# Performance work log

Hardware: AMD Instinct MI355X
Metric: run time of the kernel (lower is better)

Reference implementation:

```python
import jax, jax.numpy as jnp
import numpy as np

N_NODES = 100000
N_EDGES = 3200000
NFEAT, NHID, NCLASS = 512, 128, 40


def _glorot(key, fan_in, fan_out):
    lim = jnp.sqrt(6.0 / (fan_in + fan_out))
    return jax.random.uniform(key, (fan_in, fan_out), jnp.float32, -lim, lim)


def setup_inputs() -> dict:
    key = jax.random.key(0)
    k1, k2, k3, k4, k5 = jax.random.split(key, 5)
    x = jax.random.normal(k1, (N_NODES, NFEAT), jnp.float32)
    edge_index = jax.random.randint(k2, (2, N_EDGES), 0, N_NODES, jnp.int64)
    edge_weight = jax.random.uniform(k3, (N_EDGES,), jnp.float32)
    W1 = _glorot(k4, NFEAT, NHID)
    b1 = jnp.zeros((NHID,), jnp.float32)
    W2 = _glorot(k5, NHID, NCLASS)
    b2 = jnp.zeros((NCLASS,), jnp.float32)
    return {"x": x, "edge_index": edge_index, "edge_weight": edge_weight,
            "W1": W1, "b1": b1, "W2": W2, "b2": b2}


def _gcn_norm(edge_index, edge_weight, num_nodes):
    # add self loops (weight 1), symmetric normalization D^-1/2 A D^-1/2
    loop = jnp.arange(num_nodes, dtype=edge_index.dtype)
    row = jnp.concatenate([edge_index[0], loop])
    col = jnp.concatenate([edge_index[1], loop])
    w = jnp.concatenate([edge_weight, jnp.ones((num_nodes,), edge_weight.dtype)])
    deg = jax.ops.segment_sum(w, col, num_segments=num_nodes)
    dinv = jnp.where(deg > 0, jax.lax.rsqrt(jnp.maximum(deg, 1e-20)), 0.0)
    norm = dinv[row] * w * dinv[col]
    return row, col, norm


def _gcn_conv(h, row, col, norm, W, b, num_nodes):
    h = h @ W                                  # [N, out]
    msg = norm[:, None] * h[row]               # per-edge gather + scale
    out = jax.ops.segment_sum(msg, col, num_segments=num_nodes)  # scatter-add
    return out + b


def reference(x, edge_index, edge_weight, W1, b1, W2, b2):
    n = x.shape[0]
    row, col, norm = _gcn_norm(edge_index, edge_weight, n)
    h = jax.nn.relu(_gcn_conv(x, row, col, norm, W1, b1, n))
    # dropout: eval mode (training=False) -> identity
    return _gcn_conv(h, row, col, norm, W2, b2, n)
```

## Files before the change

kernel.cpp:

```cpp
#include <hip/hip_runtime.h>

#define NN 100000
#define NE 3200000
#define NF 512
#define NH 128
#define NC 40
#define NBIN 196
#define BINW 512
#define CAP  20480
#define EPB  4096

typedef __attribute__((ext_vector_type(8))) short bfrag;
typedef __attribute__((ext_vector_type(4))) float f32x4;
typedef __attribute__((ext_vector_type(8))) unsigned short u16x8;

static __device__ __forceinline__ unsigned short f2bf(float x) {
  unsigned u = __float_as_uint(x);
  u += 0x7FFF + ((u >> 16) & 1);
  return (unsigned short)(u >> 16);
}
static __device__ __forceinline__ float bf2f(unsigned short b) {
  return __uint_as_float(((unsigned)b) << 16);
}
static __device__ __forceinline__ float bflo(unsigned u) { return __uint_as_float(u << 16); }
static __device__ __forceinline__ float bfhi(unsigned u) { return __uint_as_float(u & 0xFFFF0000u); }


__global__ __launch_bounds__(256) void k_wconv(const float* __restrict__ W1,
                                               unsigned short* __restrict__ Wfh,
                                               unsigned short* __restrict__ Wfl,
                                               int* __restrict__ binfill) {
  if (blockIdx.x == 0 && threadIdx.x < NBIN) binfill[threadIdx.x] = 0;
  int i = blockIdx.x * 256 + threadIdx.x;
  int k = i >> 7, n = i & 127;
  float w = W1[i];
  unsigned short hi = f2bf(w);
  unsigned short lo = f2bf(w - bf2f(hi));
  int idx = ((k >> 3) * 128 + n) * 8 + (k & 7);
  Wfh[idx] = hi; Wfl[idx] = lo;
}


__global__ __launch_bounds__(256) void k_binA(const int* __restrict__ row, const int* __restrict__ col,
                                              const float* __restrict__ w,
                                              int* __restrict__ binfill, int2* __restrict__ binned) {
  __shared__ int hist[NBIN];
  __shared__ int base[NBIN];
  int t = threadIdx.x;
  int eb = blockIdx.x * EPB;
  for (int i = t; i < NBIN; i += 256) hist[i] = 0;
  __syncthreads();
  int rk[16], bn[16], sr[16]; float wv[16];
#pragma unroll
  for (int j = 0; j < 16; ++j) {
    int e = eb + t + j * 256;
    if (e < NE) {
      int c = __builtin_nontemporal_load(col + e);
      bn[j] = c >> 9;
      sr[j] = __builtin_nontemporal_load(row + e) | ((c & 511) << 17);
      wv[j] = __builtin_nontemporal_load(w + e);
      rk[j] = atomicAdd(&hist[bn[j]], 1);
    } else bn[j] = -1;
  }
  __syncthreads();
  if (t < NBIN) { int hv = hist[t]; base[t] = hv ? atomicAdd(&binfill[t], hv) : 0; }
  __syncthreads();
#pragma unroll
  for (int j = 0; j < 16; ++j) {
    if (bn[j] >= 0) {
      int pos = base[bn[j]] + rk[j];
      if (pos < CAP) binned[(size_t)bn[j] * CAP + pos] = make_int2(sr[j], __float_as_int(wv[j]));
    }
  }
}


__global__ __launch_bounds__(256) void k_binscan(const int* __restrict__ binfill,
                                                 int* __restrict__ binptr, int* __restrict__ rowptr) {
  __shared__ int sm[256];
  int t = threadIdx.x;
  sm[t] = (t < NBIN) ? binfill[t] : 0;
  __syncthreads();
  for (int off = 1; off < 256; off <<= 1) {
    int a = (t >= off) ? sm[t - off] : 0;
    __syncthreads();
    sm[t] += a;
    __syncthreads();
  }
  if (t <= NBIN) binptr[t] = (t == 0) ? 0 : sm[t - 1];
  if (t == 0) rowptr[NN] = NE;
}


__global__ __launch_bounds__(256) void k_binB(const int* __restrict__ binfill, const int* __restrict__ binptr,
                                              const int2* __restrict__ binned, int2* __restrict__ pair,
                                              int* __restrict__ rowptr, float* __restrict__ dinv) {
  __shared__ unsigned long long pk[BINW];
  __shared__ unsigned short lrank[CAP];
  __shared__ int lptr[BINW];
  __shared__ int sm[256];
  int t = threadIdx.x;
  int bin = blockIdx.x;
  int cnt = binfill[bin]; if (cnt > CAP) cnt = CAP;
  int bb = binptr[bin];
  pk[t] = 0ULL; pk[t + 256] = 0ULL;
  __syncthreads();
  const int2* src = binned + (size_t)bin * CAP;
  for (int i = t; i < cnt; i += 256) {
    int2 r = src[i];
    int lc = (unsigned)r.x >> 17;
    unsigned long long fw = (unsigned long long)(unsigned)(__int_as_float(r.y) * 16777216.0f + 0.5f);
    unsigned long long old = atomicAdd(&pk[lc], (1ULL << 42) | fw);
    lrank[i] = (unsigned short)(old >> 42);
  }
  __syncthreads();
  int c0 = (int)(pk[2 * t] >> 42), c1 = (int)(pk[2 * t + 1] >> 42);
  sm[t] = c0 + c1;
  __syncthreads();
  for (int off = 1; off < 256; off <<= 1) {
    int a = (t >= off) ? sm[t - off] : 0;
    __syncthreads();
    sm[t] += a;
    __syncthreads();
  }
  int excl = (t == 0) ? 0 : sm[t - 1];
  lptr[2 * t] = excl;
  lptr[2 * t + 1] = excl + c0;
  int n0 = bin * BINW + 2 * t;
  if (n0 < NN) {
    rowptr[n0] = bb + excl;
    float d = (float)(pk[2 * t] & 0x3FFFFFFFFFFULL) * (1.0f / 16777216.0f) + 1.0f;
    dinv[n0] = rsqrtf(d);
  }
  if (n0 + 1 < NN) {
    rowptr[n0 + 1] = bb + excl + c0;
    float d = (float)(pk[2 * t + 1] & 0x3FFFFFFFFFFULL) * (1.0f / 16777216.0f) + 1.0f;
    dinv[n0 + 1] = rsqrtf(d);
  }
  __syncthreads();
  for (int i = t; i < cnt; i += 256) {
    int2 r = src[i];
    int lc = (unsigned)r.x >> 17;
    int pos = bb + lptr[lc] + (int)lrank[i];
    pair[pos] = make_int2(r.x & 0x1FFFF, r.y);
  }
}


__global__ __launch_bounds__(256) void k_gemm1(const float* __restrict__ X,
                                               const unsigned short* __restrict__ Wfh,
                                               const unsigned short* __restrict__ Wfl,
                                               const float* __restrict__ dinv,
                                               unsigned short* __restrict__ HXb) {
  __shared__ unsigned short Ah[2][4096], Bh[2][4096], Bl[2][4096];
  int t = threadIdx.x;
  int lane = t & 63;
  int wid = t >> 6;
  int m0 = blockIdx.x * 128;
  int sm = t & 127;
  int skh = t >> 7;
  const float* xrow = X + (size_t)(m0 + sm) * NF + skh * 16;
  bool mok = (m0 + sm) < NN;
  int wm = wid >> 1, wn = wid & 1;
  int mb = wm * 64, nb = wn * 64;
  int fr = lane & 15, fg = lane >> 4;

  f32x4 acc[4][4];
#pragma unroll
  for (int i = 0; i < 4; ++i)
#pragma unroll
    for (int j = 0; j < 4; ++j) acc[i][j] = (f32x4)0.0f;

  u16x8 vb0, vb1, vc0, vc1;
  float4 xv[4];
  {
    const u16x8* sh = (const u16x8*)Wfh;
    const u16x8* sl = (const u16x8*)Wfl;
    vb0 = sh[t]; vb1 = sh[t + 256];
    vc0 = sl[t]; vc1 = sl[t + 256];
#pragma unroll
    for (int q = 0; q < 4; ++q)
      xv[q] = mok ? *(const float4*)(xrow + q * 4) : make_float4(0.f, 0.f, 0.f, 0.f);
  }

  for (int ks = 0; ks < 16; ++ks) {
    int cur = ks & 1;
#pragma unroll
    for (int q = 0; q < 4; ++q) {
      float f[4] = {xv[q].x, xv[q].y, xv[q].z, xv[q].w};
      unsigned short h[4];
#pragma unroll
      for (int j = 0; j < 4; ++j) h[j] = f2bf(f[j]);
      int lk = skh * 16 + q * 4;
      int base = ((lk >> 3) * 128 + sm) * 8 + (lk & 7);
      uint2 hv = make_uint2((unsigned)h[0] | ((unsigned)h[1] << 16),
                            (unsigned)h[2] | ((unsigned)h[3] << 16));
      *(uint2*)&Ah[cur][base] = hv;
    }
    ((u16x8*)Bh[cur])[t] = vb0; ((u16x8*)Bh[cur])[t + 256] = vb1;
    ((u16x8*)Bl[cur])[t] = vc0; ((u16x8*)Bl[cur])[t + 256] = vc1;
    if (ks < 15) {
      const u16x8* sh = (const u16x8*)(Wfh + (size_t)(ks + 1) * 4096);
      const u16x8* sl = (const u16x8*)(Wfl + (size_t)(ks + 1) * 4096);
      vb0 = sh[t]; vb1 = sh[t + 256];
      vc0 = sl[t]; vc1 = sl[t + 256];
#pragma unroll
      for (int q = 0; q < 4; ++q)
        xv[q] = mok ? *(const float4*)(xrow + (ks + 1) * 32 + q * 4)
                    : make_float4(0.f, 0.f, 0.f, 0.f);
    }
    __syncthreads();
    bfrag ah[4], bh[4], bl[4];
#pragma unroll
    for (int mi = 0; mi < 4; ++mi)
      ah[mi] = *(bfrag*)&Ah[cur][(fg * 128 + mb + mi * 16 + fr) * 8];
#pragma unroll
    for (int nt = 0; nt < 4; ++nt) {
      int idx = (fg * 128 + nb + nt * 16 + fr) * 8;
      bh[nt] = *(bfrag*)&Bh[cur][idx];
      bl[nt] = *(bfrag*)&Bl[cur][idx];
    }
#pragma unroll
    for (int mi = 0; mi < 4; ++mi)
#pragma unroll
      for (int nt = 0; nt < 4; ++nt) {
        acc[mi][nt] = __builtin_amdgcn_mfma_f32_16x16x32_bf16(ah[mi], bh[nt], acc[mi][nt], 0, 0, 0);
        acc[mi][nt] = __builtin_amdgcn_mfma_f32_16x16x32_bf16(ah[mi], bl[nt], acc[mi][nt], 0, 0, 0);
      }
  }
#pragma unroll
  for (int mi = 0; mi < 4; ++mi) {
    int rb = m0 + mb + mi * 16 + fg * 4;
#pragma unroll
    for (int q = 0; q < 4; ++q) {
      int r = rb + q;
      if (r < NN) {
        float dv = dinv[r];
#pragma unroll
        for (int nt = 0; nt < 4; ++nt) {
          int c = nb + nt * 16 + fr;
          __builtin_nontemporal_store(f2bf(dv * acc[mi][nt][q]), HXb + (size_t)r * NH + c);
        }
      }
    }
  }
}


#define FMA8(n, v)                                            \
  { unsigned uu[4] = {(v).x, (v).y, (v).z, (v).w};            \
    _Pragma("unroll")                                         \
    for (int q = 0; q < 4; ++q) {                             \
      ax[q] = fmaf((n), bflo(uu[q]), ax[q]);                  \
      ay[q] = fmaf((n), bfhi(uu[q]), ay[q]);                  \
    } }

__global__ __launch_bounds__(256) void k_agg1(const int* __restrict__ rowptr, const int2* __restrict__ pair,
                                              const unsigned* __restrict__ hxb, const float* __restrict__ dinv,
                                              const float* __restrict__ b1, unsigned* __restrict__ hb) {
  int wid = (blockIdx.x * 256 + threadIdx.x) >> 6;
  int lane = threadIdx.x & 63;
  if (wid >= NN) return;
  int sub = lane >> 4, fl = lane & 15;
  int beg = rowptr[wid], end = rowptr[wid + 1];
  const uint4* hx4 = (const uint4*)hxb;
  const long long* pr = (const long long*)pair;
  float ax[4] = {0.f, 0.f, 0.f, 0.f}, ay[4] = {0.f, 0.f, 0.f, 0.f};
  int e = beg;
  for (; e + 16 <= end; e += 16) {
    long long r0 = pr[e + sub];
    long long r1 = pr[e + 4 + sub];
    long long r2 = pr[e + 8 + sub];
    long long r3 = pr[e + 12 + sub];
    uint4 v0 = hx4[(size_t)(unsigned)(r0 & 0x1FFFF) * 16 + fl];
    uint4 v1 = hx4[(size_t)(unsigned)(r1 & 0x1FFFF) * 16 + fl];
    uint4 v2 = hx4[(size_t)(unsigned)(r2 & 0x1FFFF) * 16 + fl];
    uint4 v3 = hx4[(size_t)(unsigned)(r3 & 0x1FFFF) * 16 + fl];
    float n0 = __int_as_float((int)(r0 >> 32));
    float n1 = __int_as_float((int)(r1 >> 32));
    float n2 = __int_as_float((int)(r2 >> 32));
    float n3 = __int_as_float((int)(r3 >> 32));
    FMA8(n0, v0);
    FMA8(n1, v1);
    FMA8(n2, v2);
    FMA8(n3, v3);
  }
  for (; e + 8 <= end; e += 8) {
    long long r0 = pr[e + sub];
    long long r1 = pr[e + 4 + sub];
    uint4 v0 = hx4[(size_t)(unsigned)(r0 & 0x1FFFF) * 16 + fl];
    uint4 v1 = hx4[(size_t)(unsigned)(r1 & 0x1FFFF) * 16 + fl];
    float n0 = __int_as_float((int)(r0 >> 32));
    float n1 = __int_as_float((int)(r1 >> 32));
    FMA8(n0, v0);
    FMA8(n1, v1);
  }
  for (; e < end; e += 4) {
    int idx = e + sub;
    bool ok = idx < end;
    long long r0 = ok ? pr[idx] : 0;
    unsigned s = ok ? (unsigned)(r0 & 0x1FFFF) : (unsigned)wid;
    float n0 = ok ? __int_as_float((int)(r0 >> 32)) : 0.f;
    uint4 v0 = hx4[(size_t)s * 16 + fl];
    FMA8(n0, v0);
  }
  if (sub == 0) {
    uint4 ov = hx4[(size_t)wid * 16 + fl];
    FMA8(1.0f, ov);
  }
#pragma unroll
  for (int q = 0; q < 4; ++q) {
    ax[q] += __shfl_xor(ax[q], 16, 64); ay[q] += __shfl_xor(ay[q], 16, 64);
    ax[q] += __shfl_xor(ax[q], 32, 64); ay[q] += __shfl_xor(ay[q], 32, 64);
  }
  if (sub == 0) {
    float di = dinv[wid];
    float4 bA = ((const float4*)b1)[fl * 2];
    float4 bB = ((const float4*)b1)[fl * 2 + 1];
    float bxs[4] = {bA.x, bA.z, bB.x, bB.z};
    float bys[4] = {bA.y, bA.w, bB.y, bB.w};
    unsigned o[4];
#pragma unroll
    for (int q = 0; q < 4; ++q) {
      float rx = fmaxf(fmaf(di, ax[q], bxs[q]), 0.f);
      float ry = fmaxf(fmaf(di, ay[q], bys[q]), 0.f);
      o[q] = (unsigned)f2bf(rx) | ((unsigned)f2bf(ry) << 16);
    }
    ((uint4*)hb)[(size_t)wid * 16 + fl] = make_uint4(o[0], o[1], o[2], o[3]);
  }
}


__global__ __launch_bounds__(256) void k_gemm2(const unsigned* __restrict__ hb, const float* __restrict__ W2,
                                               const float* __restrict__ dinv,
                                               unsigned short* __restrict__ H2b) {
  __shared__ float Hs[32][132];
  __shared__ float Ws[NH * NC];
  int t = threadIdx.x;
  int m0 = blockIdx.x * 32;
  {
    int r = t >> 3, cb = (t & 7) * 8;
    int rowi = m0 + r;
    if (rowi < NN) {
      uint4 a = *(const uint4*)(hb + (size_t)rowi * 64 + cb);
      uint4 b = *(const uint4*)(hb + (size_t)rowi * 64 + cb + 4);
      unsigned u[8] = {a.x, a.y, a.z, a.w, b.x, b.y, b.z, b.w};
#pragma unroll
      for (int j = 0; j < 8; ++j) {
        Hs[r][cb * 2 + j * 2]     = bflo(u[j]);
        Hs[r][cb * 2 + j * 2 + 1] = bfhi(u[j]);
      }
    } else {
#pragma unroll
      for (int j = 0; j < 16; ++j) Hs[r][cb * 2 + j] = 0.f;
    }
  }
  for (int i = t; i < NH * NC; i += 256) Ws[i] = W2[i];
  __syncthreads();
  int r = t >> 3, c0 = (t & 7) * 5;
  float acc[5] = {0.f, 0.f, 0.f, 0.f, 0.f};
#pragma unroll 4
  for (int k = 0; k < NH; ++k) {
    float hv = Hs[r][k];
#pragma unroll
    for (int j = 0; j < 5; ++j) acc[j] = fmaf(hv, Ws[k * NC + c0 + j], acc[j]);
  }
  int rowi = m0 + r;
  if (rowi < NN) {
    float dv = dinv[rowi];
#pragma unroll
    for (int j = 0; j < 5; ++j)
      __builtin_nontemporal_store(f2bf(dv * acc[j]), H2b + (size_t)rowi * 64 + c0 + j);
    int prr = t & 7;
    if (prr < 3) {
#pragma unroll
      for (int j = 0; j < 8; ++j)
        __builtin_nontemporal_store((unsigned short)0, H2b + (size_t)rowi * 64 + 40 + prr * 8 + j);
    }
  }
}


#define FMA4(n, v)                                            \
  { unsigned uu[2] = {(v).x, (v).y};                          \
    _Pragma("unroll")                                         \
    for (int q = 0; q < 2; ++q) {                             \
      ax[q] = fmaf((n), bflo(uu[q]), ax[q]);                  \
      ay[q] = fmaf((n), bfhi(uu[q]), ay[q]);                  \
    } }

__global__ __launch_bounds__(256) void k_agg2(const int* __restrict__ rowptr, const int2* __restrict__ pair,
                                              const unsigned* __restrict__ h2u,
                                              const float* __restrict__ dinv,
                                              const float* __restrict__ b2, float* __restrict__ out) {
  int wid = (blockIdx.x * 256 + threadIdx.x) >> 6;
  int lane = threadIdx.x & 63;
  if (wid >= NN) return;
  int sub = lane >> 4, fl = lane & 15;
  int beg = rowptr[wid], end = rowptr[wid + 1];
  const uint2* h4 = (const uint2*)h2u;
  const long long* pr = (const long long*)pair;
  float ax[2] = {0.f, 0.f}, ay[2] = {0.f, 0.f};
  int e = beg;
  for (; e + 16 <= end; e += 16) {
    long long r0 = pr[e + sub];
    long long r1 = pr[e + 4 + sub];
    long long r2 = pr[e + 8 + sub];
    long long r3 = pr[e + 12 + sub];
    uint2 v0 = h4[(size_t)(unsigned)(r0 & 0x1FFFF) * 16 + fl];
    uint2 v1 = h4[(size_t)(unsigned)(r1 & 0x1FFFF) * 16 + fl];
    uint2 v2 = h4[(size_t)(unsigned)(r2 & 0x1FFFF) * 16 + fl];
    uint2 v3 = h4[(size_t)(unsigned)(r3 & 0x1FFFF) * 16 + fl];
    float n0 = __int_as_float((int)(r0 >> 32));
    float n1 = __int_as_float((int)(r1 >> 32));
    float n2 = __int_as_float((int)(r2 >> 32));
    float n3 = __int_as_float((int)(r3 >> 32));
    FMA4(n0, v0);
    FMA4(n1, v1);
    FMA4(n2, v2);
    FMA4(n3, v3);
  }
  for (; e + 8 <= end; e += 8) {
    long long r0 = pr[e + sub];
    long long r1 = pr[e + 4 + sub];
    uint2 v0 = h4[(size_t)(unsigned)(r0 & 0x1FFFF) * 16 + fl];
    uint2 v1 = h4[(size_t)(unsigned)(r1 & 0x1FFFF) * 16 + fl];
    float n0 = __int_as_float((int)(r0 >> 32));
    float n1 = __int_as_float((int)(r1 >> 32));
    FMA4(n0, v0);
    FMA4(n1, v1);
  }
  for (; e < end; e += 4) {
    int idx = e + sub;
    bool ok = idx < end;
    long long r0 = ok ? pr[idx] : 0;
    unsigned s = ok ? (unsigned)(r0 & 0x1FFFF) : (unsigned)wid;
    float n0 = ok ? __int_as_float((int)(r0 >> 32)) : 0.f;
    uint2 v0 = h4[(size_t)s * 16 + fl];
    FMA4(n0, v0);
  }
  if (sub == 0) {
    uint2 ov = h4[(size_t)wid * 16 + fl];
    FMA4(1.0f, ov);
  }
#pragma unroll
  for (int q = 0; q < 2; ++q) {
    ax[q] += __shfl_xor(ax[q], 16, 64); ay[q] += __shfl_xor(ay[q], 16, 64);
    ax[q] += __shfl_xor(ax[q], 32, 64); ay[q] += __shfl_xor(ay[q], 32, 64);
  }
  if (sub == 0 && fl < 10) {
    float di = dinv[wid];
    float4 bv = ((const float4*)b2)[fl];
    float4 o = make_float4(fmaf(di, ax[0], bv.x), fmaf(di, ay[0], bv.y),
                           fmaf(di, ax[1], bv.z), fmaf(di, ay[1], bv.w));
    *(float4*)(out + (size_t)wid * NC + fl * 4) = o;
  }
}


extern "C" void kernel_launch(void* const* d_in, const int* in_sizes, int n_in,
                              void* d_out, int out_size, void* d_ws, size_t ws_size,
                              hipStream_t stream) {
  const float* x  = (const float*)d_in[0];
  const int*   ei = (const int*)d_in[1];
  const float* ew = (const float*)d_in[2];
  const float* W1 = (const float*)d_in[3];
  const float* b1 = (const float*)d_in[4];
  const float* W2 = (const float*)d_in[5];
  const float* b2 = (const float*)d_in[6];
  float* out = (float*)d_out;
  const int* row = ei;
  const int* col = ei + NE;

  char* ws = (char*)d_ws;
  size_t o = 0;
  auto alloc = [&](size_t bytes) -> void* {
    void* p = ws + o;
    o += (bytes + 255) & ~(size_t)255;
    return p;
  };
  float* dinv    = (float*)alloc((size_t)NN * 4);
  int*   rowptr  = (int*)alloc((size_t)(NN + 1) * 4);
  int*   binfill = (int*)alloc(1024);
  int*   binptr  = (int*)alloc(1024);
  int2*  pair    = (int2*)alloc((size_t)NE * 8);
  unsigned short* Wfh = (unsigned short*)alloc((size_t)NF * NH * 2);
  unsigned short* Wfl = (unsigned short*)alloc((size_t)NF * NH * 2);
  unsigned short* hxb = (unsigned short*)alloc((size_t)NN * NH * 2);
  unsigned*       hb  = (unsigned*)alloc((size_t)NN * NH * 2);
  int2*  binned  = (int2*)alloc((size_t)NBIN * CAP * 8);
  unsigned short* h2b = (unsigned short*)hxb;

  k_wconv<<<(NF * NH) / 256, 256, 0, stream>>>(W1, Wfh, Wfl, binfill);
  k_binA<<<(NE + EPB - 1) / EPB, 256, 0, stream>>>(row, col, ew, binfill, binned);
  k_binscan<<<1, 256, 0, stream>>>(binfill, binptr, rowptr);
  k_binB<<<NBIN, 256, 0, stream>>>(binfill, binptr, binned, pair, rowptr, dinv);
  k_gemm1<<<(NN + 127) / 128, 256, 0, stream>>>(x, Wfh, Wfl, dinv, hxb);
  k_agg1<<<(NN * 64) / 256, 256, 0, stream>>>(rowptr, pair, (const unsigned*)hxb, dinv, b1, hb);
  k_gemm2<<<(NN + 31) / 32, 256, 0, stream>>>(hb, W2, dinv, h2b);
  k_agg2<<<(NN * 64) / 256, 256, 0, stream>>>(rowptr, pair, (const unsigned*)h2b, dinv, b2, out);
}
```

Baseline: 392.6 us.

## Load A fragments directly to registers in gemm1, dropping A shared-memory staging

The first GEMM's warp tiling changes from a 2x2 layout (64x64 per warp) to each warp owning 32 rows across all 128 columns. Each lane now loads its own X fragment straight from global memory and converts it to bf16 in registers, so the shared-memory A buffer and its writes and reads go away. The barrier moves earlier, before the next-tile prefetch. In exchange, B fragments are read from LDS by every warp over the full width, and global X reads become per-lane strided 32-byte chunks that may coalesce less well.

```diff
diff --git a/kernel.cpp b/kernel.cpp
--- a/kernel.cpp
+++ b/kernel.cpp
@@ -147,100 +147,91 @@
 }
 
 
+static __device__ __forceinline__ bfrag pack8(float4 lo, float4 hi) {
+  union { bfrag f; unsigned short s[8]; } u;
+  u.s[0] = f2bf(lo.x); u.s[1] = f2bf(lo.y); u.s[2] = f2bf(lo.z); u.s[3] = f2bf(lo.w);
+  u.s[4] = f2bf(hi.x); u.s[5] = f2bf(hi.y); u.s[6] = f2bf(hi.z); u.s[7] = f2bf(hi.w);
+  return u.f;
+}
+
 __global__ __launch_bounds__(256) void k_gemm1(const float* __restrict__ X,
                                                const unsigned short* __restrict__ Wfh,
                                                const unsigned short* __restrict__ Wfl,
                                                const float* __restrict__ dinv,
                                                unsigned short* __restrict__ HXb) {
-  __shared__ unsigned short Ah[2][4096], Bh[2][4096], Bl[2][4096];
+  __shared__ unsigned short Bh[2][4096], Bl[2][4096];
   int t = threadIdx.x;
   int lane = t & 63;
   int wid = t >> 6;
   int m0 = blockIdx.x * 128;
-  int sm = t & 127;
-  int skh = t >> 7;
-  const float* xrow = X + (size_t)(m0 + sm) * NF + skh * 16;
-  bool mok = (m0 + sm) < NN;
-  int wm = wid >> 1, wn = wid & 1;
-  int mb = wm * 64, nb = wn * 64;
   int fr = lane & 15, fg = lane >> 4;
-
-  f32x4 acc[4][4];
-#pragma unroll
-  for (int i = 0; i < 4; ++i)
-#pragma unroll
-    for (int j = 0; j < 4; ++j) acc[i][j] = (f32x4)0.0f;
+  int wrow = m0 + wid * 32;
+  const float* arp0 = X + (size_t)(wrow + fr) * NF + fg * 8;
+  const float* arp1 = X + (size_t)(wrow + 16 + fr) * NF + fg * 8;
+  bool ok0 = (wrow + fr) < NN;
+  bool ok1 = (wrow + 16 + fr) < NN;
+  const float4 z4 = make_float4(0.f, 0.f, 0.f, 0.f);
+
+  f32x4 acc[2][8];
+#pragma unroll
+  for (int i = 0; i < 2; ++i)
+#pragma unroll
+    for (int j = 0; j < 8; ++j) acc[i][j] = (f32x4)0.0f;
 
   u16x8 vb0, vb1, vc0, vc1;
-  float4 xv[4];
+  float4 a00, a01, a10, a11;
   {
     const u16x8* sh = (const u16x8*)Wfh;
     const u16x8* sl = (const u16x8*)Wfl;
     vb0 = sh[t]; vb1 = sh[t + 256];
     vc0 = sl[t]; vc1 = sl[t + 256];
-#pragma unroll
-    for (int q = 0; q < 4; ++q)
-      xv[q] = mok ? *(const float4*)(xrow + q * 4) : make_float4(0.f, 0.f, 0.f, 0.f);
+    a00 = ok0 ? *(const float4*)(arp0)     : z4;
+    a01 = ok0 ? *(const float4*)(arp0 + 4) : z4;
+    a10 = ok1 ? *(const float4*)(arp1)     : z4;
+    a11 = ok1 ? *(const float4*)(arp1 + 4) : z4;
   }
 
   for (int ks = 0; ks < 16; ++ks) {
     int cur = ks & 1;
-#pragma unroll
-    for (int q = 0; q < 4; ++q) {
-      float f[4] = {xv[q].x, xv[q].y, xv[q].z, xv[q].w};
-      unsigned short h[4];
-#pragma unroll
-      for (int j = 0; j < 4; ++j) h[j] = f2bf(f[j]);
-      int lk = skh * 16 + q * 4;
-      int base = ((lk >> 3) * 128 + sm) * 8 + (lk & 7);
-      uint2 hv = make_uint2((unsigned)h[0] | ((unsigned)h[1] << 16),
-                            (unsigned)h[2] | ((unsigned)h[3] << 16));
-      *(uint2*)&Ah[cur][base] = hv;
-    }
     ((u16x8*)Bh[cur])[t] = vb0; ((u16x8*)Bh[cur])[t + 256] = vb1;
     ((u16x8*)Bl[cur])[t] = vc0; ((u16x8*)Bl[cur])[t + 256] = vc1;
+    bfrag ah0 = pack8(a00, a01);
+    bfrag ah1 = pack8(a10, a11);
+    __syncthreads();
     if (ks < 15) {
       const u16x8* sh = (const u16x8*)(Wfh + (size_t)(ks + 1) * 4096);
       const u16x8* sl = (const u16x8*)(Wfl + (size_t)(ks + 1) * 4096);
       vb0 = sh[t]; vb1 = sh[t + 256];
       vc0 = sl[t]; vc1 = sl[t + 256];
-#pragma unroll
-      for (int q = 0; q < 4; ++q)
-        xv[q] = mok ? *(const float4*)(xrow + (ks + 1) * 32 + q * 4)
-                    : make_float4(0.f, 0.f, 0.f, 0.f);
-    }
-    __syncthreads();
-    bfrag ah[4], bh[4], bl[4];
-#pragma unroll
-    for (int mi = 0; mi < 4; ++mi)
-      ah[mi] = *(bfrag*)&Ah[cur][(fg * 128 + mb + mi * 16 + fr) * 8];
-#pragma unroll
-    for (int nt = 0; nt < 4; ++nt) {
-      int idx = (fg * 128 + nb + nt * 16 + fr) * 8;
-      bh[nt] = *(bfrag*)&Bh[cur][idx];
-      bl[nt] = *(bfrag*)&Bl[cur][idx];
-    }
-#pragma unroll
-    for (int mi = 0; mi < 4; ++mi)
-#pragma unroll
-      for (int nt = 0; nt < 4; ++nt) {
-        acc[mi][nt] = __builtin_amdgcn_mfma_f32_16x16x32_bf16(ah[mi], bh[nt], acc[mi][nt], 0, 0, 0);
-        acc[mi][nt] = __builtin_amdgcn_mfma_f32_16x16x32_bf16(ah[mi], bl[nt], acc[mi][nt], 0, 0, 0);
-      }
-  }
-#pragma unroll
-  for (int mi = 0; mi < 4; ++mi) {
-    int rb = m0 + mb + mi * 16 + fg * 4;
+      int ko = (ks + 1) * 32;
+      a00 = ok0 ? *(const float4*)(arp0 + ko)     : z4;
+      a01 = ok0 ? *(const float4*)(arp0 + ko + 4) : z4;
+      a10 = ok1 ? *(const float4*)(arp1 + ko)     : z4;
+      a11 = ok1 ? *(const float4*)(arp1 + ko + 4) : z4;
+    }
+#pragma unroll
+    for (int nt = 0; nt < 8; ++nt) {
+      int idx = (fg * 128 + nt * 16 + fr) * 8;
+      bfrag bh = *(bfrag*)&Bh[cur][idx];
+      bfrag bl = *(bfrag*)&Bl[cur][idx];
+      acc[0][nt] = __builtin_amdgcn_mfma_f32_16x16x32_bf16(ah0, bh, acc[0][nt], 0, 0, 0);
+      acc[1][nt] = __builtin_amdgcn_mfma_f32_16x16x32_bf16(ah1, bh, acc[1][nt], 0, 0, 0);
+      acc[0][nt] = __builtin_amdgcn_mfma_f32_16x16x32_bf16(ah0, bl, acc[0][nt], 0, 0, 0);
+      acc[1][nt] = __builtin_amdgcn_mfma_f32_16x16x32_bf16(ah1, bl, acc[1][nt], 0, 0, 0);
+    }
+  }
+#pragma unroll
+  for (int mi = 0; mi < 2; ++mi) {
+    int rb = wrow + mi * 16 + fg * 4;
 #pragma unroll
     for (int q = 0; q < 4; ++q) {
       int r = rb + q;
       if (r < NN) {
         float dv = dinv[r];
 #pragma unroll
-        for (int nt = 0; nt < 4; ++nt) {
-          int c = nb + nt * 16 + fr;
-          __builtin_nontemporal_store(f2bf(dv * acc[mi][nt][q]), HXb + (size_t)r * NH + c);
-        }
+        for (int nt = 0; nt < 8; ++nt)
+          __builtin_nontemporal_store(f2bf(dv * acc[mi][nt][q]),
+                                      HXb + (size_t)r * NH + nt * 16 + fr);
       }
     }
   }
```

After: 459.1 us. 1.17x slower.
